# Kernel tuning notes

Measured on AMD Instinct MI355X. Metric: run time of the kernel, lower is better.

The kernel has to match this reference:

```python
import jax, jax.numpy as jnp
import numpy as np

T, B, D, H = 1024, 128, 512, 256

def _linear_params(k, out_dim, in_dim):
    kw, kb = jax.random.split(k)
    s = 1.0 / np.sqrt(in_dim)
    w = jax.random.uniform(kw, (out_dim, in_dim), minval=-s, maxval=s, dtype=jnp.float32)
    b = jax.random.uniform(kb, (out_dim,), minval=-s, maxval=s, dtype=jnp.float32)
    return w, b

def setup_inputs() -> dict:
    key = jax.random.key(0)
    ks = jax.random.split(key, 9)
    x = jax.random.normal(ks[0], (T, B, D), dtype=jnp.float32)
    fc_w, fc_b = _linear_params(ks[1], H, D)
    forget_w, forget_b = _linear_params(ks[2], H, 2 * H)
    input_w, input_b = _linear_params(ks[3], H, 2 * H)
    update_w, update_b = _linear_params(ks[4], H, 2 * H)
    output_w, output_b = _linear_params(ks[5], H, 2 * H)
    cls_w0, cls_b0 = _linear_params(ks[6], H, H)
    cls_w1, cls_b1 = _linear_params(ks[7], H, H)
    cls_w2, cls_b2 = _linear_params(ks[8], 2, H)
    return dict(x=x, fc_w=fc_w, fc_b=fc_b,
                forget_w=forget_w, forget_b=forget_b,
                input_w=input_w, input_b=input_b,
                update_w=update_w, update_b=update_b,
                output_w=output_w, output_b=output_b,
                cls_w0=cls_w0, cls_b0=cls_b0,
                cls_w1=cls_w1, cls_b1=cls_b1,
                cls_w2=cls_w2, cls_b2=cls_b2)

def reference(x, fc_w, fc_b, forget_w, forget_b, input_w, input_b,
              update_w, update_b, output_w, output_b,
              cls_w0, cls_b0, cls_w1, cls_b1, cls_w2, cls_b2):
    # FC + tanh: [T,B,D] -> [T,B,H]
    h = jnp.tanh(x @ fc_w.T + fc_b)

    # LSTM-style gating over the leading time axis (state is [B,H])
    def step(carry, inp):
        hx, cx = carry
        comb = jnp.concatenate([inp, hx], axis=-1)  # [B, 2H]
        f = jax.nn.sigmoid(comb @ forget_w.T + forget_b)
        i = jax.nn.sigmoid(comb @ input_w.T + input_b)
        g = jnp.tanh(comb @ update_w.T + update_b)
        o = jax.nn.sigmoid(comb @ output_w.T + output_b)
        cx = f * cx + i * g
        hx = o * jnp.tanh(cx)
        return (hx, cx), hx

    init = (jnp.zeros((B, H), h.dtype), jnp.zeros((B, H), h.dtype))
    _, hs = jax.lax.scan(step, init, h)  # hs: [T,B,H]

    # classifier MLP (depth=2) -> 2 logits
    z = jax.nn.relu(hs @ cls_w0.T + cls_b0)
    z = jax.nn.relu(z @ cls_w1.T + cls_b1)
    return z @ cls_w2.T + cls_b2  # [T,B,2]
```

## Files before the change

### kernel.cpp

```cpp
#include <hip/hip_runtime.h>
#include <cstdint>

#define TT 1024
#define BB 128
#define DD 512
#define HH 256
#define TBR (TT*BB)

typedef __attribute__((ext_vector_type(8))) short  s8v;
typedef __attribute__((ext_vector_type(4))) float  f4v;
typedef __attribute__((ext_vector_type(4))) unsigned u4v;

__device__ __forceinline__ float sigf(float x) {
    return __builtin_amdgcn_rcpf(1.0f + __expf(-x));
}
__device__ __forceinline__ float tanh_fast(float x) {
    float e = __expf(fabsf(x) * 2.0f);
    float t = 1.0f - 2.0f * __builtin_amdgcn_rcpf(e + 1.0f);
    return copysignf(t, x);
}

__device__ __forceinline__ unsigned rnbf(float f) {
    unsigned u = __builtin_bit_cast(unsigned, f);
    return (u + 0x7FFFu + ((u >> 16) & 1u)) >> 16;
}

__global__ __launch_bounds__(256) void pack_kernel(
    const float* __restrict__ fw, const float* __restrict__ iw,
    const float* __restrict__ uw, const float* __restrict__ ow,
    const float* __restrict__ fb, const float* __restrict__ ib,
    const float* __restrict__ ub, const float* __restrict__ obb,
    float* __restrict__ wx_p, float* __restrict__ wh_p, float* __restrict__ b_p)
{
    const int r = blockIdx.x;
    const int gate = r >> 8, h = r & 255;
    const float* wsrc = gate == 0 ? fw : gate == 1 ? iw : gate == 2 ? uw : ow;
    const float* bsrc = gate == 0 ? fb : gate == 1 ? ib : gate == 2 ? ub : obb;
    const int k = threadIdx.x;
    wx_p[(size_t)r * 256 + k] = wsrc[(size_t)h * 512 + k];
    wh_p[(size_t)r * 256 + k] = wsrc[(size_t)h * 512 + 256 + k];
    if (k == 0) b_p[r] = bsrc[h];
}

__global__ __launch_bounds__(256) void pack_mfma(
    const float* __restrict__ fw, const float* __restrict__ iw,
    const float* __restrict__ uw, const float* __restrict__ ow,
    const float* __restrict__ fb, const float* __restrict__ ib,
    const float* __restrict__ ub, const float* __restrict__ obb,
    float* __restrict__ wx_p, float* __restrict__ wh_p, float* __restrict__ b_p)
{
    const int r = blockIdx.x;
    const int gate = (r >> 5) & 3;
    const int h = (r >> 7) * 32 + (r & 31);
    const float* wsrc = gate == 0 ? fw : gate == 1 ? iw : gate == 2 ? uw : ow;
    const float* bsrc = gate == 0 ? fb : gate == 1 ? ib : gate == 2 ? ub : obb;
    const int k = threadIdx.x;
    wx_p[(size_t)r * 256 + k] = wsrc[(size_t)h * 512 + k];
    wh_p[(size_t)r * 256 + k] = wsrc[(size_t)h * 512 + 256 + k];
    if (k == 0) b_p[r] = bsrc[h];
}

template<int K, int ACT, int PERM>
__global__ __launch_bounds__(256) void gemm_kernel(
    const float* A, const float* __restrict__ W,
    const float* __restrict__ bias, float* C, int N)
{
    __shared__ __align__(16) float As[16][192];
    __shared__ __align__(16) float Wt[16][192];
    const int tid = threadIdx.x;
    const int m0 = blockIdx.x * 128, n0 = blockIdx.y * 128;
    const int tm = tid >> 4, tn = tid & 15;
    const int am = tm * 12, wn = tn * 12;
    float acc[8][8] = {};
    for (int kc = 0; kc < K; kc += 16) {
        #pragma unroll
        for (int i = 0; i < 2; ++i) {
            int f4 = tid + 256 * i;
            int r = f4 >> 2, k4 = (f4 & 3) * 4;
            float4 av = *(const float4*)&A[(size_t)(m0 + r) * K + kc + k4];
            float4 wv = *(const float4*)&W[(size_t)(n0 + r) * K + kc + k4];
            int fo = (r >> 3) * 12 + (r & 7);
            As[k4 + 0][fo] = av.x; As[k4 + 1][fo] = av.y;
            As[k4 + 2][fo] = av.z; As[k4 + 3][fo] = av.w;
            Wt[k4 + 0][fo] = wv.x; Wt[k4 + 1][fo] = wv.y;
            Wt[k4 + 2][fo] = wv.z; Wt[k4 + 3][fo] = wv.w;
        }
        __syncthreads();
        #pragma unroll
        for (int kk = 0; kk < 16; ++kk) {
            float a[8], w[8];
            *(float4*)&a[0] = *(const float4*)&As[kk][am];
            *(float4*)&a[4] = *(const float4*)&As[kk][am + 4];
            *(float4*)&w[0] = *(const float4*)&Wt[kk][wn];
            *(float4*)&w[4] = *(const float4*)&Wt[kk][wn + 4];
            #pragma unroll
            for (int i = 0; i < 8; ++i)
                #pragma unroll
                for (int j = 0; j < 8; ++j)
                    acc[i][j] = fmaf(a[i], w[j], acc[i][j]);
        }
        __syncthreads();
    }
    #pragma unroll
    for (int i = 0; i < 8; ++i) {
        int m = m0 + tm * 8 + i;
        #pragma unroll
        for (int jh = 0; jh < 2; ++jh) {
            float4 v; float* vp = (float*)&v;
            #pragma unroll
            for (int l = 0; l < 4; ++l) {
                int n = n0 + tn * 8 + jh * 4 + l;
                float t = acc[i][jh * 4 + l] + bias[n];
                if (ACT == 1) t = tanhf(t);
                if (ACT == 2) t = fmaxf(t, 0.0f);
                vp[l] = t;
            }
            int nb = n0 + tn * 8 + jh * 4;
            int nc = PERM ? (((nb & 255) >> 3) * 32 + ((nb >> 8) << 3) + (nb & 7)) : nb;
            *(float4*)&C[(size_t)m * N + nc] = v;
        }
    }
}

__global__ __launch_bounds__(256, 1) void recur_mfma(
    float* __restrict__ h_buf,
    const float* __restrict__ xg,
    const float* __restrict__ wh_mf,
    unsigned long long* __restrict__ ring)
{
    __shared__ __align__(16) unsigned ldsH[16 * 128];
    __shared__ __align__(16) unsigned ldsL[16 * 128];
    __shared__ float pre[16][132];
    const int tid = threadIdx.x;
    const int lane = tid & 63;
    const int wv = tid >> 6;
    const int bg = blockIdx.x & 7, hg = blockIdx.x >> 3;
    const int b0 = bg * 16;
    const int nlo = lane & 15, quad = lane >> 4;

    s8v bh[2][8], bl[2][8];
    #pragma unroll
    for (int nt = 0; nt < 2; ++nt) {
        int r = hg * 128 + wv * 32 + nt * 16 + nlo;
        #pragma unroll
        for (int ks = 0; ks < 8; ++ks) {
            const float* src = wh_mf + (size_t)r * 256 + ks * 32 + quad * 8;
            u4v uh, ul;
            #pragma unroll
            for (int p = 0; p < 4; ++p) {
                float f0 = src[2 * p], f1 = src[2 * p + 1];
                unsigned h0 = rnbf(f0), h1 = rnbf(f1);
                float r0 = f0 - __builtin_bit_cast(float, h0 << 16);
                float r1 = f1 - __builtin_bit_cast(float, h1 << 16);
                uh[p] = h0 | (h1 << 16);
                ul[p] = rnbf(r0) | (rnbf(r1) << 16);
            }
            bh[nt][ks] = __builtin_bit_cast(s8v, uh);
            bl[nt][ks] = __builtin_bit_cast(s8v, ul);
        }
    }

    const int sm = tid >> 4;
    const int sc0 = (tid & 15) * 2;
    const int cb = tid >> 4, q = tid & 15;
    const unsigned long long SENT = ~0ull;

    float cx0 = 0.0f, cx1 = 0.0f;

    for (int t = 0; t < TT; ++t) {
        float2 xq[4];
        {
            const float* xr = xg + ((size_t)t * BB + b0 + cb) * 1024 + hg * 128 + 2 * q;
            #pragma unroll
            for (int g = 0; g < 4; ++g)
                xq[g] = *(const float2*)&xr[g * 32];
        }

        const int p0 = sm * 128 + ((sc0 ^ (sm & 7)) << 2);
        const int p1 = sm * 128 + (((sc0 + 1) ^ (sm & 7)) << 2);

        if (t == 0) {
            u4v z = {0u, 0u, 0u, 0u};
            *(u4v*)&ldsH[p0] = z; *(u4v*)&ldsH[p1] = z;
            *(u4v*)&ldsL[p0] = z; *(u4v*)&ldsL[p1] = z;
        } else {
            unsigned long long* src =
                ring + ((size_t)((t - 1) & 3) * 128 + b0 + sm) * 128 + sc0 * 4;
            unsigned long long a[8];
            long bud = 1L << 22;
            for (;;) {
                #pragma unroll
                for (int i = 0; i < 8; ++i)
                    a[i] = __hip_atomic_load(&src[i], __ATOMIC_RELAXED,
                                             __HIP_MEMORY_SCOPE_AGENT);
                bool ok = true;
                #pragma unroll
                for (int i = 0; i < 8; ++i) ok = ok && (a[i] != SENT);
                if (__all(ok)) break;
                if (--bud < 0) break;
                __builtin_amdgcn_s_sleep(1);
            }
            u4v w0 = { (unsigned)a[0], (unsigned)a[1], (unsigned)a[2], (unsigned)a[3] };
            u4v w1 = { (unsigned)a[4], (unsigned)a[5], (unsigned)a[6], (unsigned)a[7] };
            u4v v0 = { (unsigned)(a[0] >> 32), (unsigned)(a[1] >> 32),
                       (unsigned)(a[2] >> 32), (unsigned)(a[3] >> 32) };
            u4v v1 = { (unsigned)(a[4] >> 32), (unsigned)(a[5] >> 32),
                       (unsigned)(a[6] >> 32), (unsigned)(a[7] >> 32) };
            *(u4v*)&ldsH[p0] = w0; *(u4v*)&ldsH[p1] = w1;
            *(u4v*)&ldsL[p0] = v0; *(u4v*)&ldsL[p1] = v1;

            if (t >= 2) {
                __hip_atomic_store(
                    &ring[((size_t)((t - 2) & 3) * 128 + b0 + cb) * 128 + hg * 16 + q],
                    SENT, __ATOMIC_RELAXED, __HIP_MEMORY_SCOPE_AGENT);
            }
        }
        __syncthreads();

        f4v acc0 = {0.f, 0.f, 0.f, 0.f}, acc1 = {0.f, 0.f, 0.f, 0.f};
        #pragma unroll
        for (int ks = 0; ks < 8; ++ks) {
            int off = nlo * 128 + ((((ks * 4 + quad) ^ (nlo & 7))) << 2);
            s8v ah = __builtin_bit_cast(s8v, *(const u4v*)&ldsH[off]);
            s8v al = __builtin_bit_cast(s8v, *(const u4v*)&ldsL[off]);
            acc0 = __builtin_amdgcn_mfma_f32_16x16x32_bf16(ah, bh[0][ks], acc0, 0, 0, 0);
            acc1 = __builtin_amdgcn_mfma_f32_16x16x32_bf16(ah, bh[1][ks], acc1, 0, 0, 0);
            acc0 = __builtin_amdgcn_mfma_f32_16x16x32_bf16(al, bh[0][ks], acc0, 0, 0, 0);
            acc1 = __builtin_amdgcn_mfma_f32_16x16x32_bf16(al, bh[1][ks], acc1, 0, 0, 0);
            acc0 = __builtin_amdgcn_mfma_f32_16x16x32_bf16(ah, bl[0][ks], acc0, 0, 0, 0);
            acc1 = __builtin_amdgcn_mfma_f32_16x16x32_bf16(ah, bl[1][ks], acc1, 0, 0, 0);
        }
        {
            int n0c = wv * 32 + nlo;
            #pragma unroll
            for (int reg = 0; reg < 4; ++reg) {
                pre[quad * 4 + reg][n0c]      = acc0[reg];
                pre[quad * 4 + reg][n0c + 16] = acc1[reg];
            }
        }
        __syncthreads();

        float2 pf = *(const float2*)&pre[cb][0 * 32 + 2 * q];
        float2 pi = *(const float2*)&pre[cb][1 * 32 + 2 * q];
        float2 pg = *(const float2*)&pre[cb][2 * 32 + 2 * q];
        float2 po = *(const float2*)&pre[cb][3 * 32 + 2 * q];
        float f0 = sigf(pf.x + xq[0].x), f1 = sigf(pf.y + xq[0].y);
        float i0 = sigf(pi.x + xq[1].x), i1 = sigf(pi.y + xq[1].y);
        float g0 = tanh_fast(pg.x + xq[2].x), g1 = tanh_fast(pg.y + xq[2].y);
        float o0 = sigf(po.x + xq[3].x), o1 = sigf(po.y + xq[3].y);
        cx0 = f0 * cx0 + i0 * g0;
        cx1 = f1 * cx1 + i1 * g1;
        float hv0 = o0 * tanh_fast(cx0);
        float hv1 = o1 * tanh_fast(cx1);

        unsigned hb0 = rnbf(hv0), hb1 = rnbf(hv1);
        float l0 = hv0 - __builtin_bit_cast(float, hb0 << 16);
        float l1 = hv1 - __builtin_bit_cast(float, hb1 << 16);
        unsigned long long atom =
            (unsigned long long)(hb0 | (hb1 << 16)) |
            ((unsigned long long)(rnbf(l0) | (rnbf(l1) << 16)) << 32);
        __hip_atomic_store(
            &ring[((size_t)(t & 3) * 128 + b0 + cb) * 128 + hg * 16 + q],
            atom, __ATOMIC_RELAXED, __HIP_MEMORY_SCOPE_AGENT);
        *(float2*)&h_buf[((size_t)t * BB + b0 + cb) * 256 + hg * 32 + 2 * q] =
            make_float2(hv0, hv1);
    }
}

__device__ __forceinline__ int swz(int row, int k4) {
    return row * 256 + (((k4 ^ (row & 7)) & 63) << 2);
}

__global__ __launch_bounds__(256, 1) void recur_kernel(
    float* h_buf, const float* __restrict__ xg,
    const float* __restrict__ wx_p, const float* __restrict__ wh_p,
    const float* __restrict__ b_p, float* hx_buf, int* flags, int use_xg)
{
    __shared__ __align__(16) float Ws[32 * 256];
    __shared__ __align__(16) float Ss[32 * 256];
    const int tid = threadIdx.x;
    const int lane = tid & 63;
    const int bg = blockIdx.x & 3, hg = blockIdx.x >> 2;
    const int b0 = bg * 32;
    const int b = tid >> 3, h = tid & 7;
    const int wrow = tid >> 3;
    const int wkb = (tid & 7) * 32;

    float bias0 = b_p[0 * 256 + hg * 8 + h];
    float bias1 = b_p[1 * 256 + hg * 8 + h];
    float bias2 = b_p[2 * 256 + hg * 8 + h];
    float bias3 = b_p[3 * 256 + hg * 8 + h];
    __syncthreads();

    float cx = 0.0f, pv = 0.0f;

    for (int t = 0; t < TT; ++t) {
        if (t > 0) {
            const int* fp = flags + (size_t)(t - 1) * 128 + bg * 32 + (lane & 31);
            long bud = 1L << 22;
            for (;;) {
                int v = __hip_atomic_load(fp, __ATOMIC_RELAXED, __HIP_MEMORY_SCOPE_AGENT);
                if (__all(v != 0)) break;
                if (--bud < 0) break;
                __builtin_amdgcn_s_sleep(1);
            }
        }
        float acc0, acc1, acc2, acc3;
        {
            if (t > 0)
                h_buf[((size_t)(t - 1) * BB + b0 + b) * 256 + hg * 8 + h] = pv;
            acc0 = bias0; acc1 = bias1; acc2 = bias2; acc3 = bias3;
            {
                const int R = (wrow >> 3) * 256 + hg * 8 + (wrow & 7);
                const float* src = wx_p + (size_t)R * 256 + wkb;
                #pragma unroll
                for (int j = 0; j < 8; ++j)
                    *(float4*)&Ws[swz(wrow, (wkb >> 2) + j)] = *(const float4*)&src[j * 4];
                const float* hs = h_buf + ((size_t)t * BB + b0) * HH;
                #pragma unroll
                for (int i = 0; i < 32; ++i)
                    Ss[i * 256 + ((((tid >> 2) ^ (i & 7)) & 63) << 2) + (tid & 3)] =
                        hs[i * 256 + tid];
            }
            __syncthreads();
            #pragma unroll 4
            for (int k4 = 0; k4 < 64; ++k4) {
                float4 s  = *(const float4*)&Ss[swz(b, k4)];
                float4 w0 = *(const float4*)&Ws[(0 * 8 + h) * 256 + (((k4 ^ h) & 63) << 2)];
                float4 w1 = *(const float4*)&Ws[(1 * 8 + h) * 256 + (((k4 ^ h) & 63) << 2)];
                float4 w2 = *(const float4*)&Ws[(2 * 8 + h) * 256 + (((k4 ^ h) & 63) << 2)];
                float4 w3 = *(const float4*)&Ws[(3 * 8 + h) * 256 + (((k4 ^ h) & 63) << 2)];
                acc0 += s.x*w0.x + s.y*w0.y + s.z*w0.z + s.w*w0.w;
                acc1 += s.x*w1.x + s.y*w1.y + s.z*w1.z + s.w*w1.w;
                acc2 += s.x*w2.x + s.y*w2.y + s.z*w2.z + s.w*w2.w;
                acc3 += s.x*w3.x + s.y*w3.y + s.z*w3.z + s.w*w3.w;
            }
            __syncthreads();
            {
                const int R = (wrow >> 3) * 256 + hg * 8 + (wrow & 7);
                const float* src = wh_p + (size_t)R * 256 + wkb;
                #pragma unroll
                for (int j = 0; j < 8; ++j)
                    *(float4*)&Ws[swz(wrow, (wkb >> 2) + j)] = *(const float4*)&src[j * 4];
            }
        }
        {
            const float* hxr = hx_buf + (size_t)(t & 1) * (BB * HH) + (size_t)b0 * HH;
            #pragma unroll
            for (int i = 0; i < 32; ++i) {
                float v = __hip_atomic_load(&hxr[i * 256 + tid],
                                            __ATOMIC_RELAXED, __HIP_MEMORY_SCOPE_AGENT);
                Ss[i * 256 + ((((tid >> 2) ^ (i & 7)) & 63) << 2) + (tid & 3)] = v;
            }
        }
        __syncthreads();
        #pragma unroll 4
        for (int k4 = 0; k4 < 64; ++k4) {
            float4 s  = *(const float4*)&Ss[swz(b, k4)];
            float4 w0 = *(const float4*)&Ws[(0 * 8 + h) * 256 + (((k4 ^ h) & 63) << 2)];
            float4 w1 = *(const float4*)&Ws[(1 * 8 + h) * 256 + (((k4 ^ h) & 63) << 2)];
            float4 w2 = *(const float4*)&Ws[(2 * 8 + h) * 256 + (((k4 ^ h) & 63) << 2)];
            float4 w3 = *(const float4*)&Ws[(3 * 8 + h) * 256 + (((k4 ^ h) & 63) << 2)];
            acc0 += s.x*w0.x + s.y*w0.y + s.z*w0.z + s.w*w0.w;
            acc1 += s.x*w1.x + s.y*w1.y + s.z*w1.z + s.w*w1.w;
            acc2 += s.x*w2.x + s.y*w2.y + s.z*w2.z + s.w*w2.w;
            acc3 += s.x*w3.x + s.y*w3.y + s.z*w3.z + s.w*w3.w;
        }
        __syncthreads();

        float fg = sigf(acc0), ig = sigf(acc1), gg = tanhf(acc2), og = sigf(acc3);
        cx = fg * cx + ig * gg;
        float hxv = og * tanhf(cx);
        pv = hxv;

        __hip_atomic_store(
            &hx_buf[(size_t)((t + 1) & 1) * (BB * HH) + (size_t)(b0 + b) * HH + hg * 8 + h],
            hxv, __ATOMIC_RELAXED, __HIP_MEMORY_SCOPE_AGENT);
        asm volatile("s_waitcnt vmcnt(0)" ::: "memory");
        __syncthreads();
        if (tid == 0)
            __hip_atomic_store(&flags[(size_t)t * 128 + bg * 32 + hg], 1,
                               __ATOMIC_RELAXED, __HIP_MEMORY_SCOPE_AGENT);
    }

    {
        const int* fp = flags + (size_t)1023 * 128 + bg * 32 + (lane & 31);
        long bud = 1L << 22;
        for (;;) {
            int v = __hip_atomic_load(fp, __ATOMIC_RELAXED, __HIP_MEMORY_SCOPE_AGENT);
            if (__all(v != 0)) break;
            if (--bud < 0) break;
            __builtin_amdgcn_s_sleep(1);
        }
        h_buf[((size_t)1023 * BB + b0 + b) * 256 + hg * 8 + h] = pv;
    }
}

__global__ __launch_bounds__(256) void final_kernel(
    const float* __restrict__ z, const float* __restrict__ w2,
    const float* __restrict__ b2, float* __restrict__ out)
{
    const int m = blockIdx.x * 128 + (threadIdx.x >> 1);
    const int c = threadIdx.x & 1;
    const float* zr = z + (size_t)m * 256;
    const float* wr = w2 + (size_t)c * 256;
    float s = b2[c];
    #pragma unroll 8
    for (int k = 0; k < 256; k += 4) {
        float4 zv = *(const float4*)&zr[k];
        float4 wv = *(const float4*)&wr[k];
        s += zv.x*wv.x + zv.y*wv.y + zv.z*wv.z + zv.w*wv.w;
    }
    out[(size_t)m * 2 + c] = s;
}

extern "C" void kernel_launch(void* const* d_in, const int* in_sizes, int n_in,
                              void* d_out, int out_size, void* d_ws, size_t ws_size,
                              hipStream_t stream) {
    const float* x    = (const float*)d_in[0];
    const float* fc_w = (const float*)d_in[1];
    const float* fc_b = (const float*)d_in[2];
    const float* fw   = (const float*)d_in[3];
    const float* fb   = (const float*)d_in[4];
    const float* iw   = (const float*)d_in[5];
    const float* ib   = (const float*)d_in[6];
    const float* uw   = (const float*)d_in[7];
    const float* ub   = (const float*)d_in[8];
    const float* ow   = (const float*)d_in[9];
    const float* ob   = (const float*)d_in[10];
    const float* w0   = (const float*)d_in[11];
    const float* b0   = (const float*)d_in[12];
    const float* w1   = (const float*)d_in[13];
    const float* b1   = (const float*)d_in[14];
    const float* w2   = (const float*)d_in[15];
    const float* b2   = (const float*)d_in[16];
    float* out = (float*)d_out;

    float* ws = (float*)d_ws;
    size_t off = 0;
    float* h_buf  = ws + off; off += (size_t)TBR * HH;
    float* wx_p   = ws + off; off += 1024 * 256;
    float* wh_p   = ws + off; off += 1024 * 256;
    float* b_p    = ws + off; off += 1024;
    float* hx_buf = ws + off; off += 2 * BB * HH;
    float* sync_f = ws + off; off += 131072;
    const size_t base_f = off;
    float* xg = ws + base_f;
    const size_t need_xg = (base_f + (size_t)TBR * 1024) * sizeof(float);
    const int use_xg = (ws_size >= need_xg) ? 1 : 0;
    float* z0 = use_xg ? xg : (ws + base_f);

    if (use_xg) {
        hipMemsetAsync(sync_f, 0xFF, 131072 * sizeof(float), stream);
        pack_mfma<<<1024, 256, 0, stream>>>(fw, iw, uw, ow, fb, ib, ub, ob,
                                            wx_p, wh_p, b_p);
        gemm_kernel<512, 1, 0><<<dim3(TBR / 128, 2), 256, 0, stream>>>(
            x, fc_w, fc_b, h_buf, 256);
        gemm_kernel<256, 0, 0><<<dim3(TBR / 128, 8), 256, 0, stream>>>(
            h_buf, wx_p, b_p, xg, 1024);
        recur_mfma<<<64, 256, 0, stream>>>(h_buf, xg, wh_p,
                                           (unsigned long long*)sync_f);
    } else {
        hipMemsetAsync(hx_buf, 0, (2 * BB * HH + 131072) * sizeof(float), stream);
        pack_kernel<<<1024, 256, 0, stream>>>(fw, iw, uw, ow, fb, ib, ub, ob,
                                              wx_p, wh_p, b_p);
        gemm_kernel<512, 1, 0><<<dim3(TBR / 128, 2), 256, 0, stream>>>(
            x, fc_w, fc_b, h_buf, 256);
        recur_kernel<<<128, 256, 0, stream>>>(h_buf, nullptr, wx_p, wh_p, b_p,
                                              hx_buf, (int*)sync_f, 0);
    }
    gemm_kernel<256, 2, 0><<<dim3(TBR / 128, 2), 256, 0, stream>>>(
        h_buf, w0, b0, z0, 256);
    gemm_kernel<256, 2, 0><<<dim3(TBR / 128, 2), 256, 0, stream>>>(
        z0, w1, b1, h_buf, 256);
    final_kernel<<<TBR / 128, 256, 0, stream>>>(h_buf, w2, b2, out);
}
```

Baseline: 4.687 ms.

## Fuse input-gate projection into recurrent MFMA kernel, dropping xg precompute GEMM

Removes the separate GEMM that precomputed the input projection (xg, T*B*1024 floats) and instead computes it inside the recurrent kernel each step with split-bf16 MFMAs. Weights for the input part are held in registers, and the FC output for the next step is prefetched while the current step runs. This avoids writing and re-reading a large intermediate buffer and one kernel launch. In exchange it adds MFMA work and register pressure inside the latency-bound serial recurrence, where the input part can overlap the wait on the ring.

```diff
diff --git a/kernel.cpp b/kernel.cpp
--- a/kernel.cpp
+++ b/kernel.cpp
@@ -124,12 +124,16 @@
 
 __global__ __launch_bounds__(256, 1) void recur_mfma(
     float* __restrict__ h_buf,
-    const float* __restrict__ xg,
+    const float* __restrict__ hfc,
+    const float* __restrict__ wx_mf,
     const float* __restrict__ wh_mf,
+    const float* __restrict__ b_mf,
     unsigned long long* __restrict__ ring)
 {
     __shared__ __align__(16) unsigned ldsH[16 * 128];
     __shared__ __align__(16) unsigned ldsL[16 * 128];
+    __shared__ __align__(16) unsigned ldsXH[16 * 128];
+    __shared__ __align__(16) unsigned ldsXL[16 * 128];
     __shared__ float pre[16][132];
     const int tid = threadIdx.x;
     const int lane = tid & 63;
@@ -139,45 +143,93 @@
     const int nlo = lane & 15, quad = lane >> 4;
 
     s8v bh[2][8], bl[2][8];
-    #pragma unroll
-    for (int nt = 0; nt < 2; ++nt) {
-        int r = hg * 128 + wv * 32 + nt * 16 + nlo;
-        #pragma unroll
-        for (int ks = 0; ks < 8; ++ks) {
-            const float* src = wh_mf + (size_t)r * 256 + ks * 32 + quad * 8;
-            u4v uh, ul;
-            #pragma unroll
-            for (int p = 0; p < 4; ++p) {
-                float f0 = src[2 * p], f1 = src[2 * p + 1];
-                unsigned h0 = rnbf(f0), h1 = rnbf(f1);
-                float r0 = f0 - __builtin_bit_cast(float, h0 << 16);
-                float r1 = f1 - __builtin_bit_cast(float, h1 << 16);
-                uh[p] = h0 | (h1 << 16);
-                ul[p] = rnbf(r0) | (rnbf(r1) << 16);
-            }
-            bh[nt][ks] = __builtin_bit_cast(s8v, uh);
-            bl[nt][ks] = __builtin_bit_cast(s8v, ul);
-        }
-    }
+    s8v ch[2][8], cl[2][8];
+#define PACK_FRAGS(SRCPTR, BH, BL)                                            \
+    _Pragma("unroll")                                                         \
+    for (int nt = 0; nt < 2; ++nt) {                                          \
+        int r = hg * 128 + wv * 32 + nt * 16 + nlo;                           \
+        _Pragma("unroll")                                                     \
+        for (int ks = 0; ks < 8; ++ks) {                                      \
+            const float* src = SRCPTR + (size_t)r * 256 + ks * 32 + quad * 8; \
+            u4v uh, ul;                                                       \
+            _Pragma("unroll")                                                 \
+            for (int p = 0; p < 4; ++p) {                                     \
+                float f0 = src[2 * p], f1 = src[2 * p + 1];                   \
+                unsigned h0 = rnbf(f0), h1 = rnbf(f1);                        \
+                float r0 = f0 - __builtin_bit_cast(float, h0 << 16);          \
+                float r1 = f1 - __builtin_bit_cast(float, h1 << 16);          \
+                uh[p] = h0 | (h1 << 16);                                      \
+                ul[p] = rnbf(r0) | (rnbf(r1) << 16);                          \
+            }                                                                 \
+            BH[nt][ks] = __builtin_bit_cast(s8v, uh);                         \
+            BL[nt][ks] = __builtin_bit_cast(s8v, ul);                         \
+        }                                                                     \
+    }
+    PACK_FRAGS(wh_mf, bh, bl)
+    PACK_FRAGS(wx_mf, ch, cl)
+#undef PACK_FRAGS
 
     const int sm = tid >> 4;
     const int sc0 = (tid & 15) * 2;
     const int cb = tid >> 4, q = tid & 15;
     const unsigned long long SENT = ~0ull;
 
+    float bsf[4][2];
+    #pragma unroll
+    for (int g = 0; g < 4; ++g) {
+        bsf[g][0] = b_mf[hg * 128 + g * 32 + 2 * q];
+        bsf[g][1] = b_mf[hg * 128 + g * 32 + 2 * q + 1];
+    }
+
+    const int p0 = sm * 128 + ((sc0 ^ (sm & 7)) << 2);
+    const int p1 = sm * 128 + (((sc0 + 1) ^ (sm & 7)) << 2);
+
+    float4 xf[4];
+    {
+        const float* xr = hfc + ((size_t)0 * BB + b0 + sm) * 256 + (tid & 15) * 16;
+        xf[0] = *(const float4*)&xr[0];
+        xf[1] = *(const float4*)&xr[4];
+        xf[2] = *(const float4*)&xr[8];
+        xf[3] = *(const float4*)&xr[12];
+    }
+
     float cx0 = 0.0f, cx1 = 0.0f;
 
     for (int t = 0; t < TT; ++t) {
-        float2 xq[4];
         {
-            const float* xr = xg + ((size_t)t * BB + b0 + cb) * 1024 + hg * 128 + 2 * q;
+            const float* fv = (const float*)xf;
+            u4v xh0, xl0, xh1, xl1;
             #pragma unroll
-            for (int g = 0; g < 4; ++g)
-                xq[g] = *(const float2*)&xr[g * 32];
-        }
-
-        const int p0 = sm * 128 + ((sc0 ^ (sm & 7)) << 2);
-        const int p1 = sm * 128 + (((sc0 + 1) ^ (sm & 7)) << 2);
+            for (int p = 0; p < 4; ++p) {
+                float f0 = fv[2 * p], f1 = fv[2 * p + 1];
+                unsigned h0 = rnbf(f0), h1 = rnbf(f1);
+                xh0[p] = h0 | (h1 << 16);
+                xl0[p] = rnbf(f0 - __builtin_bit_cast(float, h0 << 16)) |
+                         (rnbf(f1 - __builtin_bit_cast(float, h1 << 16)) << 16);
+                float g0 = fv[8 + 2 * p], g1 = fv[8 + 2 * p + 1];
+                unsigned k0 = rnbf(g0), k1 = rnbf(g1);
+                xh1[p] = k0 | (k1 << 16);
+                xl1[p] = rnbf(g0 - __builtin_bit_cast(float, k0 << 16)) |
+                         (rnbf(g1 - __builtin_bit_cast(float, k1 << 16)) << 16);
+            }
+            *(u4v*)&ldsXH[p0] = xh0; *(u4v*)&ldsXH[p1] = xh1;
+            *(u4v*)&ldsXL[p0] = xl0; *(u4v*)&ldsXL[p1] = xl1;
+        }
+        __syncthreads();
+
+        f4v acc0 = {0.f, 0.f, 0.f, 0.f}, acc1 = {0.f, 0.f, 0.f, 0.f};
+        #pragma unroll
+        for (int ks = 0; ks < 8; ++ks) {
+            int off = nlo * 128 + ((((ks * 4 + quad) ^ (nlo & 7))) << 2);
+            s8v ah = __builtin_bit_cast(s8v, *(const u4v*)&ldsXH[off]);
+            s8v al = __builtin_bit_cast(s8v, *(const u4v*)&ldsXL[off]);
+            acc0 = __builtin_amdgcn_mfma_f32_16x16x32_bf16(ah, ch[0][ks], acc0, 0, 0, 0);
+            acc1 = __builtin_amdgcn_mfma_f32_16x16x32_bf16(ah, ch[1][ks], acc1, 0, 0, 0);
+            acc0 = __builtin_amdgcn_mfma_f32_16x16x32_bf16(al, ch[0][ks], acc0, 0, 0, 0);
+            acc1 = __builtin_amdgcn_mfma_f32_16x16x32_bf16(al, ch[1][ks], acc1, 0, 0, 0);
+            acc0 = __builtin_amdgcn_mfma_f32_16x16x32_bf16(ah, cl[0][ks], acc0, 0, 0, 0);
+            acc1 = __builtin_amdgcn_mfma_f32_16x16x32_bf16(ah, cl[1][ks], acc1, 0, 0, 0);
+        }
 
         if (t == 0) {
             u4v z = {0u, 0u, 0u, 0u};
@@ -208,16 +260,23 @@
                        (unsigned)(a[6] >> 32), (unsigned)(a[7] >> 32) };
             *(u4v*)&ldsH[p0] = w0; *(u4v*)&ldsH[p1] = w1;
             *(u4v*)&ldsL[p0] = v0; *(u4v*)&ldsL[p1] = v1;
-
             if (t >= 2) {
                 __hip_atomic_store(
                     &ring[((size_t)((t - 2) & 3) * 128 + b0 + cb) * 128 + hg * 16 + q],
                     SENT, __ATOMIC_RELAXED, __HIP_MEMORY_SCOPE_AGENT);
             }
         }
-        __syncthreads();
-
-        f4v acc0 = {0.f, 0.f, 0.f, 0.f}, acc1 = {0.f, 0.f, 0.f, 0.f};
+
+        {
+            int tn2 = (t + 1 < TT) ? (t + 1) : (TT - 1);
+            const float* xr = hfc + ((size_t)tn2 * BB + b0 + sm) * 256 + (tid & 15) * 16;
+            xf[0] = *(const float4*)&xr[0];
+            xf[1] = *(const float4*)&xr[4];
+            xf[2] = *(const float4*)&xr[8];
+            xf[3] = *(const float4*)&xr[12];
+        }
+        __syncthreads();
+
         #pragma unroll
         for (int ks = 0; ks < 8; ++ks) {
             int off = nlo * 128 + ((((ks * 4 + quad) ^ (nlo & 7))) << 2);
@@ -244,10 +303,10 @@
         float2 pi = *(const float2*)&pre[cb][1 * 32 + 2 * q];
         float2 pg = *(const float2*)&pre[cb][2 * 32 + 2 * q];
         float2 po = *(const float2*)&pre[cb][3 * 32 + 2 * q];
-        float f0 = sigf(pf.x + xq[0].x), f1 = sigf(pf.y + xq[0].y);
-        float i0 = sigf(pi.x + xq[1].x), i1 = sigf(pi.y + xq[1].y);
-        float g0 = tanh_fast(pg.x + xq[2].x), g1 = tanh_fast(pg.y + xq[2].y);
-        float o0 = sigf(po.x + xq[3].x), o1 = sigf(po.y + xq[3].y);
+        float f0 = sigf(pf.x + bsf[0][0]), f1 = sigf(pf.y + bsf[0][1]);
+        float i0 = sigf(pi.x + bsf[1][0]), i1 = sigf(pi.y + bsf[1][1]);
+        float g0 = tanh_fast(pg.x + bsf[2][0]), g1 = tanh_fast(pg.y + bsf[2][1]);
+        float o0 = sigf(po.x + bsf[3][0]), o1 = sigf(po.y + bsf[3][1]);
         cx0 = f0 * cx0 + i0 * g0;
         cx1 = f1 * cx1 + i1 * g1;
         float hv0 = o0 * tanh_fast(cx0);
@@ -445,20 +504,18 @@
     float* hx_buf = ws + off; off += 2 * BB * HH;
     float* sync_f = ws + off; off += 131072;
     const size_t base_f = off;
-    float* xg = ws + base_f;
-    const size_t need_xg = (base_f + (size_t)TBR * 1024) * sizeof(float);
-    const int use_xg = (ws_size >= need_xg) ? 1 : 0;
-    float* z0 = use_xg ? xg : (ws + base_f);
-
-    if (use_xg) {
+    float* hfc = ws + base_f;
+    const size_t need = (base_f + (size_t)TBR * 256) * sizeof(float);
+    const int use_mfma = (ws_size >= need) ? 1 : 0;
+    float* z0 = ws + base_f;
+
+    if (use_mfma) {
         hipMemsetAsync(sync_f, 0xFF, 131072 * sizeof(float), stream);
         pack_mfma<<<1024, 256, 0, stream>>>(fw, iw, uw, ow, fb, ib, ub, ob,
                                             wx_p, wh_p, b_p);
         gemm_kernel<512, 1, 0><<<dim3(TBR / 128, 2), 256, 0, stream>>>(
-            x, fc_w, fc_b, h_buf, 256);
-        gemm_kernel<256, 0, 0><<<dim3(TBR / 128, 8), 256, 0, stream>>>(
-            h_buf, wx_p, b_p, xg, 1024);
-        recur_mfma<<<64, 256, 0, stream>>>(h_buf, xg, wh_p,
+            x, fc_w, fc_b, hfc, 256);
+        recur_mfma<<<64, 256, 0, stream>>>(h_buf, hfc, wx_p, wh_p, b_p,
                                            (unsigned long long*)sync_f);
     } else {
         hipMemsetAsync(hx_buf, 0, (2 * BB * HH + 131072) * sizeof(float), stream);
```

New measurement: 4.485 ms. 1.05x faster.
